# Kernel optimization log

Measured on AMD Instinct MI355X. Metric: run time of the kernel, lower is better.

## Reference

```python
import jax, jax.numpy as jnp
import numpy as np

B, T, C = 1, 4096, 2048
NH, HS, NQG = 16, 128, 4          # n_head, head_size, n_query_groups (GQA)
Q_PER_KV = NH // NQG              # 4
QKV_DIM = (NH + 2 * NQG) * HS     # 3072
ROT = HS // 2                     # rotary half-dim = 64


def setup_inputs() -> dict:
    key = jax.random.key(0)
    k0, k1, k2 = jax.random.split(key, 3)
    x = jax.random.normal(k0, (B, T, C), dtype=jnp.float32)
    W_attn = jax.random.normal(k1, (QKV_DIM, C), dtype=jnp.float32) * 0.02
    W_proj = jax.random.normal(k2, (C, C), dtype=jnp.float32) * 0.02
    # RoPE cache: cos/sin of shape (T, head_size/2), flash-attn convention
    inv_freq = 1.0 / (10000.0 ** (jnp.arange(0, HS, 2, dtype=jnp.float32) / HS))
    freqs = jnp.arange(T, dtype=jnp.float32)[:, None] * inv_freq[None, :]
    return {"x": x, "cos": jnp.cos(freqs), "sin": jnp.sin(freqs),
            "W_attn": W_attn, "W_proj": W_proj}


def _apply_rope(t, cos, sin):
    # t: (B, T, H, HS); cos/sin: (T, ROT). Non-interleaved (rotate-half) form.
    x1, x2 = t[..., :ROT], t[..., ROT:]
    c = cos[None, :, None, :]
    s = sin[None, :, None, :]
    return jnp.concatenate([x1 * c - x2 * s, x2 * c + x1 * s], axis=-1)


def reference(x, cos, sin, W_attn, W_proj):
    Bx, Tx, Cx = x.shape
    qkv = jnp.einsum('btc,fc->btf', x, W_attn)                 # (B,T,3072)
    qkv = qkv.reshape(Bx, Tx, NQG, Q_PER_KV + 2, HS)
    q = qkv[:, :, :, :Q_PER_KV, :].reshape(Bx, Tx, NH, HS)     # (B,T,16,128)
    k = qkv[:, :, :, Q_PER_KV, :]                              # (B,T,4,128)
    v = qkv[:, :, :, Q_PER_KV + 1, :]                          # (B,T,4,128)
    q = _apply_rope(q, cos, sin)
    k = _apply_rope(k, cos, sin)
    # GQA: expand kv groups to match query heads (repeat_interleave on head dim)
    k = jnp.repeat(k, Q_PER_KV, axis=2)                        # (B,T,16,128)
    v = jnp.repeat(v, Q_PER_KV, axis=2)
    scale = 1.0 / np.sqrt(HS).astype(np.float32)
    scores = jnp.einsum('bthd,bshd->bhts', q, k) * scale       # (B,H,T,T)
    causal = jnp.tril(jnp.ones((Tx, Tx), dtype=bool))
    scores = jnp.where(causal[None, None], scores, jnp.finfo(scores.dtype).min)
    attn = jax.nn.softmax(scores, axis=-1)
    y = jnp.einsum('bhts,bshd->bthd', attn, v).reshape(Bx, Tx, Cx)
    return jnp.einsum('btc,oc->bto', y, W_proj)
```

## Files before the change

kernel.cpp:

```cpp
#include <hip/hip_runtime.h>
#include <hip/hip_bf16.h>

typedef __hip_bfloat16 bf16;
typedef __attribute__((ext_vector_type(8))) short short8;
typedef __attribute__((ext_vector_type(4))) short short4v;
typedef __attribute__((ext_vector_type(4))) float floatx4;

#define T_SEQ 4096
#define C_DIM 2048
#define NHEAD 16
#define HSZ   128
#define NGRP  4

#define MFMA_BF16(A,B,C) __builtin_amdgcn_mfma_f32_16x16x32_bf16((A),(B),(C),0,0,0)

__device__ __forceinline__ void gld_lds16(const bf16* g, bf16* l) {
  __builtin_amdgcn_global_load_lds(
      (__attribute__((address_space(1))) void*)(g),
      (__attribute__((address_space(3))) void*)(l), 16, 0, 0);
}

__global__ void cvt_kernel(const float* __restrict__ src, bf16* __restrict__ dst, long n)
{
  const long i = ((long)blockIdx.x * blockDim.x + threadIdx.x) * 8;
  if (i >= n) return;
  const float4 a = *(const float4*)(src + i);
  const float4 b = *(const float4*)(src + i + 4);
  bf16 tmp[8];
  tmp[0] = __float2bfloat16(a.x); tmp[1] = __float2bfloat16(a.y);
  tmp[2] = __float2bfloat16(a.z); tmp[3] = __float2bfloat16(a.w);
  tmp[4] = __float2bfloat16(b.x); tmp[5] = __float2bfloat16(b.y);
  tmp[6] = __float2bfloat16(b.z); tmp[7] = __float2bfloat16(b.w);
  *(short8*)(dst + i) = *(const short8*)tmp;
}

__global__ __launch_bounds__(256, 2)
void gemm_bt_kernel(const bf16* __restrict__ A, const bf16* __restrict__ B,
                    float* __restrict__ Cf, bf16* __restrict__ Cq,
                    bf16* __restrict__ Ck, bf16* __restrict__ Cvt,
                    int K, int qkv_mode)
{
  __shared__ alignas(16) bf16 As[128 * 64];
  __shared__ alignas(16) bf16 Bs[128 * 64];

  const int t  = threadIdx.x;
  const int w  = t >> 6, l = t & 63;
  const int wr = w >> 1, wc = w & 1;
  const int q4 = l >> 4, ln = l & 15;
  const long bm = (long)blockIdx.y * 128;
  const long bn = (long)blockIdx.x * 128;

  floatx4 acc[4][4] = {};

  const bf16* Ab = A + (bm + t / 8) * (long)K + (t % 8) * 8;
  const bf16* Bb = B + (bn + t / 8) * (long)K + (t % 8) * 8;

  for (int k0 = 0; k0 < K; k0 += 64) {
    __syncthreads();
#pragma unroll
    for (int i = 0; i < 4; ++i) {
      gld_lds16(Ab + (long)i * 32 * K + k0, As + (i * 256 + w * 64) * 8);
      gld_lds16(Bb + (long)i * 32 * K + k0, Bs + (i * 256 + w * 64) * 8);
    }
    __syncthreads();
#pragma unroll
    for (int kk = 0; kk < 64; kk += 32) {
      short8 af[4], bfr[4];
      const int co = kk + q4 * 8;
#pragma unroll
      for (int mi = 0; mi < 4; ++mi)
        af[mi] = *(const short8*)(As + (wr * 64 + mi * 16 + ln) * 64 + co);
#pragma unroll
      for (int ni = 0; ni < 4; ++ni)
        bfr[ni] = *(const short8*)(Bs + (wc * 64 + ni * 16 + ln) * 64 + co);
#pragma unroll
      for (int mi = 0; mi < 4; ++mi)
#pragma unroll
        for (int ni = 0; ni < 4; ++ni)
          acc[mi][ni] = MFMA_BF16(af[mi], bfr[ni], acc[mi][ni]);
    }
  }

  if (!qkv_mode) {
#pragma unroll
    for (int mi = 0; mi < 4; ++mi) {
      const long r0 = bm + wr * 64 + mi * 16 + q4 * 4;
#pragma unroll
      for (int ni = 0; ni < 4; ++ni) {
        const long c = bn + wc * 64 + ni * 16 + ln;
#pragma unroll
        for (int r = 0; r < 4; ++r)
          Cf[(r0 + r) * C_DIM + c] = acc[mi][ni][r];
      }
    }
  } else {
    const int cb = blockIdx.x;
    const int g = cb / 6, slot = cb - g * 6;
    if (slot == 5) {
      bf16* dstv = Cvt + (long)g * HSZ * T_SEQ;
#pragma unroll
      for (int mi = 0; mi < 4; ++mi) {
        const long r0 = bm + wr * 64 + mi * 16 + q4 * 4;
#pragma unroll
        for (int ni = 0; ni < 4; ++ni) {
          const long c = wc * 64 + ni * 16 + ln;
          short4v pk;
#pragma unroll
          for (int r = 0; r < 4; ++r) {
            bf16 v = __float2bfloat16(acc[mi][ni][r]);
            pk[r] = *(short*)&v;
          }
          *(short4v*)(dstv + c * T_SEQ + r0) = pk;
        }
      }
    } else {
      bf16* dst = (slot < 4) ? (Cq + (long)(g * 4 + slot) * T_SEQ * HSZ)
                             : (Ck + (long)g * T_SEQ * HSZ);
#pragma unroll
      for (int mi = 0; mi < 4; ++mi) {
        const long r0 = bm + wr * 64 + mi * 16 + q4 * 4;
#pragma unroll
        for (int ni = 0; ni < 4; ++ni) {
          const long c = wc * 64 + ni * 16 + ln;
#pragma unroll
          for (int r = 0; r < 4; ++r)
            dst[(r0 + r) * HSZ + c] = __float2bfloat16(acc[mi][ni][r]);
        }
      }
    }
  }
}

__global__ void rope_kernel(bf16* __restrict__ Q, bf16* __restrict__ Kb,
                            const float* __restrict__ cs, const float* __restrict__ sn)
{
  const long idx = (long)blockIdx.x * blockDim.x + threadIdx.x;
  const long NQ = (long)NHEAD * T_SEQ * 64;
  bf16* buf; long rem; float qs;
  if (idx < NQ) { buf = Q;  rem = idx;      qs = 0.08838834764831845f * 1.4426950408889634f; }
  else          { buf = Kb; rem = idx - NQ; qs = 1.0f; }
  const int d  = (int)(rem & 63);
  const int tt = (int)((rem >> 6) & (T_SEQ - 1));
  const int hh = (int)(rem >> 18);
  const float c = cs[tt * 64 + d];
  const float s = sn[tt * 64 + d];
  bf16* p = buf + ((long)hh * T_SEQ + tt) * HSZ + d;
  const float x1 = __bfloat162float(p[0]);
  const float x2 = __bfloat162float(p[64]);
  p[0]  = __float2bfloat16((x1 * c - x2 * s) * qs);
  p[64] = __float2bfloat16((x2 * c + x1 * s) * qs);
}

__global__ __launch_bounds__(256, 2)
void attn_kernel(const bf16* __restrict__ Qg, const bf16* __restrict__ Kg,
                 const bf16* __restrict__ Vtg, bf16* __restrict__ Y)
{
  __shared__ alignas(16) bf16 Ks[64][132];
  __shared__ alignas(16) bf16 Vt[128][68];
  __shared__ alignas(16) bf16 Ps[128][68];

  const int h = blockIdx.y;
  const int p = (blockIdx.y < 8) ? blockIdx.x : (31 - blockIdx.x);
  const int g = h >> 2;
  const int t = threadIdx.x;
  const int w = t >> 6, l = t & 63;
  const int q4 = l >> 4, ln = l & 15;

  const bf16* Qh = Qg + (long)h * T_SEQ * HSZ;
  const bf16* Kh = Kg + (long)g * T_SEQ * HSZ;
  const bf16* Vh = Vtg + (long)g * HSZ * T_SEQ;

  const int qbase = p * 128 + w * 32;

  short8 qf[2][4];
#pragma unroll
  for (int mi = 0; mi < 2; ++mi) {
    const long row = qbase + mi * 16 + ln;
#pragma unroll
    for (int ks = 0; ks < 4; ++ks)
      qf[mi][ks] = *(const short8*)(Qh + row * HSZ + ks * 32 + q4 * 8);
  }

  short8 ones_f;
#pragma unroll
  for (int i = 0; i < 8; ++i) ones_f[i] = (ln == 0) ? (short)0x3F80 : (short)0;

  floatx4 acc[2][8] = {};
  floatx4 acc_l[2] = {};

  const int krow = t >> 4, kc = (t & 15) * 8;
  const int vrow = t >> 3, vc = (t & 7) * 8;

  short8 kpre[4], vpre[4];
#pragma unroll
  for (int i = 0; i < 4; ++i) {
    kpre[i] = *(const short8*)(Kh + (long)(krow + 16 * i) * HSZ + kc);
    vpre[i] = *(const short8*)(Vh + (long)(vrow + 32 * i) * T_SEQ + vc);
  }

  const int jmax = 2 * p + 1;
  for (int j = 0; j <= jmax; ++j) {
    const int s0 = j * 64;
#pragma unroll
    for (int i = 0; i < 4; ++i) {
      *(short8*)(&Ks[krow + 16 * i][kc]) = kpre[i];
      *(short8*)(&Vt[vrow + 32 * i][vc]) = vpre[i];
    }
    __syncthreads();
    if (j < jmax) {
      const int s1 = s0 + 64;
#pragma unroll
      for (int i = 0; i < 4; ++i) {
        kpre[i] = *(const short8*)(Kh + (long)(s1 + krow + 16 * i) * HSZ + kc);
        vpre[i] = *(const short8*)(Vh + (long)(vrow + 32 * i) * T_SEQ + s1 + vc);
      }
    }

    floatx4 sacc[2][4] = {};
#pragma unroll
    for (int ks = 0; ks < 4; ++ks) {
      short8 kf[4];
#pragma unroll
      for (int ni = 0; ni < 4; ++ni)
        kf[ni] = *(const short8*)(&Ks[ni * 16 + ln][ks * 32 + q4 * 8]);
#pragma unroll
      for (int mi = 0; mi < 2; ++mi)
#pragma unroll
        for (int ni = 0; ni < 4; ++ni)
          sacc[mi][ni] = MFMA_BF16(qf[mi][ks], kf[ni], sacc[mi][ni]);
    }

#pragma unroll
    for (int mi = 0; mi < 2; ++mi) {
      const int base_m = qbase + mi * 16 + q4 * 4 - s0 - ln;
#pragma unroll
      for (int ni = 0; ni < 4; ++ni)
#pragma unroll
        for (int r = 0; r < 4; ++r) {
          float pv = __builtin_amdgcn_exp2f(sacc[mi][ni][r]);
          if (base_m + r - ni * 16 < 0) pv = 0.f;
          Ps[w * 32 + mi * 16 + q4 * 4 + r][ni * 16 + ln] = __float2bfloat16(pv);
        }
    }

#pragma unroll
    for (int ks = 0; ks < 2; ++ks) {
      short8 pf[2], vf[8];
#pragma unroll
      for (int mi = 0; mi < 2; ++mi)
        pf[mi] = *(const short8*)(&Ps[w * 32 + mi * 16 + ln][ks * 32 + q4 * 8]);
#pragma unroll
      for (int nd = 0; nd < 8; ++nd)
        vf[nd] = *(const short8*)(&Vt[nd * 16 + ln][ks * 32 + q4 * 8]);
#pragma unroll
      for (int mi = 0; mi < 2; ++mi) {
        acc_l[mi] = MFMA_BF16(pf[mi], ones_f, acc_l[mi]);
#pragma unroll
        for (int nd = 0; nd < 8; ++nd)
          acc[mi][nd] = MFMA_BF16(pf[mi], vf[nd], acc[mi][nd]);
      }
    }
    __syncthreads();
  }

#pragma unroll
  for (int mi = 0; mi < 2; ++mi) {
#pragma unroll
    for (int r = 0; r < 4; ++r) {
      const float lv = __shfl(acc_l[mi][r], l & 48, 64);
      const float inv = (lv > 0.f) ? 1.f / lv : 0.f;
      const long tq = qbase + mi * 16 + q4 * 4 + r;
#pragma unroll
      for (int nd = 0; nd < 8; ++nd)
        Y[tq * C_DIM + h * HSZ + nd * 16 + ln] = __float2bfloat16(acc[mi][nd][r] * inv);
    }
  }
}

extern "C" void kernel_launch(void* const* d_in, const int* in_sizes, int n_in,
                              void* d_out, int out_size, void* d_ws, size_t ws_size,
                              hipStream_t stream)
{
  const float* x  = (const float*)d_in[0];
  const float* cs = (const float*)d_in[1];
  const float* sn = (const float*)d_in[2];
  const float* Wa = (const float*)d_in[3];
  const float* Wp = (const float*)d_in[4];
  float* out = (float*)d_out;

  const long nx  = (long)T_SEQ * C_DIM;
  const long nwa = (long)(NHEAD + 2 * NGRP) * HSZ * C_DIM;
  const long nwp = (long)C_DIM * C_DIM;
  const long nqh = (long)NHEAD * T_SEQ * HSZ;
  const long nkg = (long)NGRP * T_SEQ * HSZ;

  const size_t need = (size_t)(nx + nwa + nqh + 2 * nkg + nqh) * sizeof(bf16);
  if (ws_size < need) return;

  bf16* xb  = (bf16*)d_ws;
  bf16* Wab = xb + nx;
  bf16* Q   = Wab + nwa;
  bf16* K   = Q + nqh;
  bf16* Vt  = K + nkg;
  bf16* Y   = Vt + nkg;
  bf16* Wpb = xb;

  cvt_kernel<<<(int)(nx  / 8 / 256), 256, 0, stream>>>(x,  xb,  nx);
  cvt_kernel<<<(int)(nwa / 8 / 256), 256, 0, stream>>>(Wa, Wab, nwa);
  gemm_bt_kernel<<<dim3(24, 32), 256, 0, stream>>>(xb, Wab, nullptr, Q, K, Vt, C_DIM, 1);
  rope_kernel<<<20480, 256, 0, stream>>>(Q, K, cs, sn);
  attn_kernel<<<dim3(32, NHEAD), 256, 0, stream>>>(Q, K, Vt, Y);
  cvt_kernel<<<(int)(nwp / 8 / 256), 256, 0, stream>>>(Wp, Wpb, nwp);
  gemm_bt_kernel<<<dim3(16, 32), 256, 0, stream>>>(Y, Wpb, out, nullptr, nullptr, nullptr, C_DIM, 0);
}
```

Before: 349.7 us.

## Rewrite attention inner loop with 32x32 MFMA, register-resident P and async LDS double buffering

The attention kernel now uses 32x32x16 MFMA tiles and computes S transposed, so each lane holds the probabilities for its own query row. P is packed to bf16 and exchanged across half-waves with a shuffle instead of being staged through LDS. The row sum is now accumulated with scalar adds instead of a ones-vector MFMA. K and V tiles are loaded asynchronously straight into double-buffered, XOR-swizzled LDS, so one barrier per iteration replaces two, and waves skip tiles that are fully masked. The GEMM launch bound occupancy hint also rises from 2 to 3, which may add register pressure.

```diff
diff --git a/kernel.cpp b/kernel.cpp
--- a/kernel.cpp
+++ b/kernel.cpp
@@ -5,6 +5,7 @@
 typedef __attribute__((ext_vector_type(8))) short short8;
 typedef __attribute__((ext_vector_type(4))) short short4v;
 typedef __attribute__((ext_vector_type(4))) float floatx4;
+typedef __attribute__((ext_vector_type(16))) float floatx16;
 
 #define T_SEQ 4096
 #define C_DIM 2048
@@ -13,11 +14,18 @@
 #define NGRP  4
 
 #define MFMA_BF16(A,B,C) __builtin_amdgcn_mfma_f32_16x16x32_bf16((A),(B),(C),0,0,0)
+#define MFMA32(A,B,C)    __builtin_amdgcn_mfma_f32_32x32x16_bf16((A),(B),(C),0,0,0)
 
 __device__ __forceinline__ void gld_lds16(const bf16* g, bf16* l) {
   __builtin_amdgcn_global_load_lds(
       (__attribute__((address_space(1))) void*)(g),
       (__attribute__((address_space(3))) void*)(l), 16, 0, 0);
+}
+
+__device__ __forceinline__ unsigned pkbf(float a, float b) {
+  bf16 x = __float2bfloat16(a), y = __float2bfloat16(b);
+  unsigned short ux = *(unsigned short*)&x, uy = *(unsigned short*)&y;
+  return ((unsigned)uy << 16) | ux;
 }
 
 __global__ void cvt_kernel(const float* __restrict__ src, bf16* __restrict__ dst, long n)
@@ -34,7 +42,7 @@
   *(short8*)(dst + i) = *(const short8*)tmp;
 }
 
-__global__ __launch_bounds__(256, 2)
+__global__ __launch_bounds__(256, 3)
 void gemm_bt_kernel(const bf16* __restrict__ A, const bf16* __restrict__ B,
                     float* __restrict__ Cf, bf16* __restrict__ Cq,
                     bf16* __restrict__ Ck, bf16* __restrict__ Cvt,
@@ -155,125 +163,127 @@
 void attn_kernel(const bf16* __restrict__ Qg, const bf16* __restrict__ Kg,
                  const bf16* __restrict__ Vtg, bf16* __restrict__ Y)
 {
-  __shared__ alignas(16) bf16 Ks[64][132];
-  __shared__ alignas(16) bf16 Vt[128][68];
-  __shared__ alignas(16) bf16 Ps[128][68];
+  __shared__ alignas(16) bf16 KS[2][64 * 128];
+  __shared__ alignas(16) bf16 VT[2][128 * 64];
 
   const int h = blockIdx.y;
-  const int p = (blockIdx.y < 8) ? blockIdx.x : (31 - blockIdx.x);
+  const int p = (blockIdx.y < 8) ? blockIdx.x : (31 - (int)blockIdx.x);
   const int g = h >> 2;
   const int t = threadIdx.x;
   const int w = t >> 6, l = t & 63;
-  const int q4 = l >> 4, ln = l & 15;
+  const int q32 = l & 31, hi = l >> 5;
+  const int k7 = q32 & 7;
 
   const bf16* Qh = Qg + (long)h * T_SEQ * HSZ;
   const bf16* Kh = Kg + (long)g * T_SEQ * HSZ;
   const bf16* Vh = Vtg + (long)g * HSZ * T_SEQ;
 
   const int qbase = p * 128 + w * 32;
-
-  short8 qf[2][4];
-#pragma unroll
-  for (int mi = 0; mi < 2; ++mi) {
-    const long row = qbase + mi * 16 + ln;
-#pragma unroll
-    for (int ks = 0; ks < 4; ++ks)
-      qf[mi][ks] = *(const short8*)(Qh + row * HSZ + ks * 32 + q4 * 8);
-  }
-
-  short8 ones_f;
-#pragma unroll
-  for (int i = 0; i < 8; ++i) ones_f[i] = (ln == 0) ? (short)0x3F80 : (short)0;
-
-  floatx4 acc[2][8] = {};
-  floatx4 acc_l[2] = {};
-
-  const int krow = t >> 4, kc = (t & 15) * 8;
-  const int vrow = t >> 3, vc = (t & 7) * 8;
-
-  short8 kpre[4], vpre[4];
+  const int qrow  = qbase + q32;
+
+  short8 qf[8];
+#pragma unroll
+  for (int kd = 0; kd < 8; ++kd)
+    qf[kd] = *(const short8*)(Qh + (long)qrow * HSZ + kd * 16 + hi * 8);
+
+  floatx16 oacc[4] = {};
+  float lacc = 0.f;
+
+  const int kr = l >> 4, ksl = l & 15;
+  const int vr = l >> 3, vsl = l & 7;
+
+  const int jmax = 2 * p + 1;
+
 #pragma unroll
   for (int i = 0; i < 4; ++i) {
-    kpre[i] = *(const short8*)(Kh + (long)(krow + 16 * i) * HSZ + kc);
-    vpre[i] = *(const short8*)(Vh + (long)(vrow + 32 * i) * T_SEQ + vc);
-  }
-
-  const int jmax = 2 * p + 1;
+    const int m = w * 4 + i;
+    const int krow = 4 * m + kr;
+    gld_lds16(Kh + (long)krow * HSZ + ((ksl ^ (krow & 7)) * 8), KS[0] + m * 512);
+    const int vrow = 8 * m + vr;
+    gld_lds16(Vh + (long)vrow * T_SEQ + ((vsl ^ vr) * 8), VT[0] + m * 512);
+  }
+
   for (int j = 0; j <= jmax; ++j) {
+    __syncthreads();
     const int s0 = j * 64;
-#pragma unroll
-    for (int i = 0; i < 4; ++i) {
-      *(short8*)(&Ks[krow + 16 * i][kc]) = kpre[i];
-      *(short8*)(&Vt[vrow + 32 * i][vc]) = vpre[i];
-    }
-    __syncthreads();
+    const bf16* KsB = KS[j & 1];
+    const bf16* VtB = VT[j & 1];
+
     if (j < jmax) {
+      bf16* ksb = KS[(j + 1) & 1];
+      bf16* vtb = VT[(j + 1) & 1];
       const int s1 = s0 + 64;
 #pragma unroll
       for (int i = 0; i < 4; ++i) {
-        kpre[i] = *(const short8*)(Kh + (long)(s1 + krow + 16 * i) * HSZ + kc);
-        vpre[i] = *(const short8*)(Vh + (long)(vrow + 32 * i) * T_SEQ + s1 + vc);
-      }
-    }
-
-    floatx4 sacc[2][4] = {};
-#pragma unroll
-    for (int ks = 0; ks < 4; ++ks) {
-      short8 kf[4];
-#pragma unroll
-      for (int ni = 0; ni < 4; ++ni)
-        kf[ni] = *(const short8*)(&Ks[ni * 16 + ln][ks * 32 + q4 * 8]);
-#pragma unroll
-      for (int mi = 0; mi < 2; ++mi)
-#pragma unroll
-        for (int ni = 0; ni < 4; ++ni)
-          sacc[mi][ni] = MFMA_BF16(qf[mi][ks], kf[ni], sacc[mi][ni]);
-    }
-
-#pragma unroll
-    for (int mi = 0; mi < 2; ++mi) {
-      const int base_m = qbase + mi * 16 + q4 * 4 - s0 - ln;
-#pragma unroll
-      for (int ni = 0; ni < 4; ++ni)
-#pragma unroll
-        for (int r = 0; r < 4; ++r) {
-          float pv = __builtin_amdgcn_exp2f(sacc[mi][ni][r]);
-          if (base_m + r - ni * 16 < 0) pv = 0.f;
-          Ps[w * 32 + mi * 16 + q4 * 4 + r][ni * 16 + ln] = __float2bfloat16(pv);
+        const int m = w * 4 + i;
+        const int krow = 4 * m + kr;
+        gld_lds16(Kh + (long)(s1 + krow) * HSZ + ((ksl ^ (krow & 7)) * 8), ksb + m * 512);
+        const int vrow = 8 * m + vr;
+        gld_lds16(Vh + (long)vrow * T_SEQ + s1 + ((vsl ^ vr) * 8), vtb + m * 512);
+      }
+    }
+
+    if (s0 > qbase + 31) continue;
+
+    floatx16 st[2] = {};
+#pragma unroll
+    for (int kd = 0; kd < 8; ++kd) {
+      const int co = ((kd * 2 + hi) ^ k7) * 8;
+      const short8 ka0 = *(const short8*)(KsB + q32 * 128 + co);
+      const short8 ka1 = *(const short8*)(KsB + (32 + q32) * 128 + co);
+      st[0] = MFMA32(ka0, qf[kd], st[0]);
+      st[1] = MFMA32(ka1, qf[kd], st[1]);
+    }
+
+    const bool domask = (s0 + 63 > qbase);
+#pragma unroll
+    for (int si = 0; si < 2; ++si) {
+      float pe[16];
+#pragma unroll
+      for (int r = 0; r < 16; ++r) {
+        float v = __builtin_amdgcn_exp2f(st[si][r]);
+        if (domask) {
+          const int sg = s0 + si * 32 + (r & 3) + 8 * (r >> 2) + 4 * hi;
+          if (sg > qrow) v = 0.f;
         }
-    }
-
-#pragma unroll
-    for (int ks = 0; ks < 2; ++ks) {
-      short8 pf[2], vf[8];
-#pragma unroll
-      for (int mi = 0; mi < 2; ++mi)
-        pf[mi] = *(const short8*)(&Ps[w * 32 + mi * 16 + ln][ks * 32 + q4 * 8]);
-#pragma unroll
-      for (int nd = 0; nd < 8; ++nd)
-        vf[nd] = *(const short8*)(&Vt[nd * 16 + ln][ks * 32 + q4 * 8]);
-#pragma unroll
-      for (int mi = 0; mi < 2; ++mi) {
-        acc_l[mi] = MFMA_BF16(pf[mi], ones_f, acc_l[mi]);
-#pragma unroll
-        for (int nd = 0; nd < 8; ++nd)
-          acc[mi][nd] = MFMA_BF16(pf[mi], vf[nd], acc[mi][nd]);
-      }
-    }
-    __syncthreads();
-  }
-
-#pragma unroll
-  for (int mi = 0; mi < 2; ++mi) {
-#pragma unroll
-    for (int r = 0; r < 4; ++r) {
-      const float lv = __shfl(acc_l[mi][r], l & 48, 64);
-      const float inv = (lv > 0.f) ? 1.f / lv : 0.f;
-      const long tq = qbase + mi * 16 + q4 * 4 + r;
-#pragma unroll
-      for (int nd = 0; nd < 8; ++nd)
-        Y[tq * C_DIM + h * HSZ + nd * 16 + ln] = __float2bfloat16(acc[mi][nd][r] * inv);
-    }
+        pe[r] = v;
+        lacc += v;
+      }
+#pragma unroll
+      for (int k2 = 0; k2 < 2; ++k2) {
+        const int ks = si * 2 + k2;
+        const int ub = 8 * k2;
+        const unsigned pw0 = pkbf(pe[ub + 0], pe[ub + 1]);
+        const unsigned pw1 = pkbf(pe[ub + 2], pe[ub + 3]);
+        const unsigned pw2 = pkbf(pe[ub + 4], pe[ub + 5]);
+        const unsigned pw3 = pkbf(pe[ub + 6], pe[ub + 7]);
+        const unsigned sx0 = (unsigned)__shfl_xor((int)(hi ? pw0 : pw2), 32, 64);
+        const unsigned sx1 = (unsigned)__shfl_xor((int)(hi ? pw1 : pw3), 32, 64);
+        union { unsigned u4[4]; short8 s8; } pa;
+        pa.u4[0] = hi ? sx0 : pw0;
+        pa.u4[1] = hi ? sx1 : pw1;
+        pa.u4[2] = hi ? pw2 : sx0;
+        pa.u4[3] = hi ? pw3 : sx1;
+        const int co = ((ks * 2 + hi) ^ k7) * 8;
+#pragma unroll
+        for (int ni = 0; ni < 4; ++ni) {
+          const short8 vb = *(const short8*)(VtB + (ni * 32 + q32) * 64 + co);
+          oacc[ni] = MFMA32(pa.s8, vb, oacc[ni]);
+        }
+      }
+    }
+  }
+
+  const float lt = lacc + __shfl_xor(lacc, 32, 64);
+#pragma unroll
+  for (int r = 0; r < 16; ++r) {
+    const int qloc = (r & 3) + 8 * (r >> 2) + 4 * hi;
+    const float dv = __shfl(lt, qloc, 64);
+    const float inv = (dv > 0.f) ? 1.f / dv : 0.f;
+    bf16* yp = Y + (long)(qbase + qloc) * C_DIM + h * HSZ + q32;
+#pragma unroll
+    for (int ni = 0; ni < 4; ++ni)
+      yp[ni * 32] = __float2bfloat16(oacc[ni][r] * inv);
   }
 }
 
```

Measured after the change: 365.3 us. 1.04x slower.
